# Kernel optimization log

Hardware: AMD Instinct MI355X
Metric: run time of the kernel (lower is better)

The kernel has to match this reference:

```python
import jax, jax.numpy as jnp
import numpy as np

N_NODES = 50000
IN_CH = 256
HID_CH = 64
N_EDGES = 800000


def setup_inputs() -> dict:
    key = jax.random.key(0)
    k1, k2, k3, k4, k5 = jax.random.split(key, 5)
    x = jax.random.normal(k1, (N_NODES, IN_CH), dtype=jnp.float32)
    edge_index = jax.random.randint(k2, (2, N_EDGES), 0, N_NODES, dtype=jnp.int64)
    # GCNConv linear weight (Glorot) and zero bias, as in PyG defaults
    W = jax.random.normal(k3, (IN_CH, HID_CH), dtype=jnp.float32) * (1.0 / np.sqrt(IN_CH))
    bias = jnp.zeros((HID_CH,), dtype=jnp.float32)
    # PReLU per-channel weight, torch default init 0.25
    prelu_a = jnp.full((HID_CH,), 0.25, dtype=jnp.float32)
    return {"x": x, "edge_index": edge_index, "W": W, "bias": bias, "prelu_a": prelu_a}


def reference(x, edge_index, W, bias, prelu_a):
    # GCNConv, normalize=False: transform then scatter-add over edges, + bias
    xw = x @ W                               # [N, H]
    src, dst = edge_index[0], edge_index[1]
    msgs = xw[src]                           # [E, H] gather
    agg = jax.ops.segment_sum(msgs, dst, num_segments=N_NODES)  # [N, H]
    out = agg + bias
    # per-channel PReLU
    return jnp.where(out > 0, out, prelu_a * out)
```

## Files before the change

kernel.cpp:

```cpp
#include <hip/hip_runtime.h>

#define N_NODES 50000
#define IN_CH   256
#define HID_CH  64
#define N_EDGES 800000

#define AG_ROWS 64
#define NBUCKET 782
#define CAPB    1536
#define PTILE   4096
#define NPT     196
#define GEMM_BLOCKS 391
#define CAP     2048

typedef __attribute__((ext_vector_type(8))) short short8;
typedef __attribute__((ext_vector_type(4))) float f32x4;

static __device__ __forceinline__ unsigned short f2bf(float f) {
    unsigned int u = __float_as_uint(f);
    u += 0x7FFF + ((u >> 16) & 1);
    return (unsigned short)(u >> 16);
}
static __device__ __forceinline__ float bf2f(unsigned short h) {
    return __uint_as_float(((unsigned int)h) << 16);
}

union SmemU {
    short8 wfl[2048];
    struct {
        int hcnt[NBUCKET];
        int excl[NBUCKET];
        int lcur[NBUCKET];
        int gbase[NBUCKET];
        int wsum[8];
        unsigned int staged[PTILE];
        unsigned short sbkt[PTILE];
    } p;
};

__global__ __launch_bounds__(512) void gemm_part_kernel(const float* __restrict__ x,
                                                        const float* __restrict__ W,
                                                        unsigned short* __restrict__ xwb,
                                                        const int* __restrict__ ei,
                                                        int* __restrict__ cnt,
                                                        unsigned int* __restrict__ packed_out) {
    __shared__ SmemU u;
    const int t = threadIdx.x;

    if (blockIdx.x < GEMM_BLOCKS) {
        for (int e = t; e < 2048; e += 512) {
            const int ks = e >> 8;
            const int nt = (e >> 6) & 3;
            const int l  = e & 63;
            const int q = l >> 4, m = l & 15;
            const int n = nt * 16 + m;
            const int k0 = ks * 32 + q * 8;
            short8 v;
            #pragma unroll
            for (int j = 0; j < 8; ++j) v[j] = (short)f2bf(W[(k0 + j) * HID_CH + n]);
            u.wfl[e] = v;
        }
        __syncthreads();

        const int wv = t >> 6, lane = t & 63;
        const int q = lane >> 4, m = lane & 15;
        const int row0 = blockIdx.x * 128 + wv * 16;
        const int arow = row0 + m;
        const int arl = arow < N_NODES ? arow : N_NODES - 1;
        const float* xr = x + (size_t)arl * IN_CH + q * 8;

        f32x4 acc0 = {0.f,0.f,0.f,0.f}, acc1 = acc0, acc2 = acc0, acc3 = acc0;

        #pragma unroll
        for (int ks = 0; ks < 8; ++ks) {
            const float4 a0 = *(const float4*)(xr + ks * 32);
            const float4 a1 = *(const float4*)(xr + ks * 32 + 4);
            short8 af;
            af[0] = (short)f2bf(a0.x); af[1] = (short)f2bf(a0.y);
            af[2] = (short)f2bf(a0.z); af[3] = (short)f2bf(a0.w);
            af[4] = (short)f2bf(a1.x); af[5] = (short)f2bf(a1.y);
            af[6] = (short)f2bf(a1.z); af[7] = (short)f2bf(a1.w);
            const short8 b0 = u.wfl[(ks * 4 + 0) * 64 + lane];
            const short8 b1 = u.wfl[(ks * 4 + 1) * 64 + lane];
            const short8 b2 = u.wfl[(ks * 4 + 2) * 64 + lane];
            const short8 b3 = u.wfl[(ks * 4 + 3) * 64 + lane];
            acc0 = __builtin_amdgcn_mfma_f32_16x16x32_bf16(af, b0, acc0, 0, 0, 0);
            acc1 = __builtin_amdgcn_mfma_f32_16x16x32_bf16(af, b1, acc1, 0, 0, 0);
            acc2 = __builtin_amdgcn_mfma_f32_16x16x32_bf16(af, b2, acc2, 0, 0, 0);
            acc3 = __builtin_amdgcn_mfma_f32_16x16x32_bf16(af, b3, acc3, 0, 0, 0);
        }

        #pragma unroll
        for (int r = 0; r < 4; ++r) {
            const int row = row0 + q * 4 + r;
            if (row < N_NODES) {
                unsigned short* o = xwb + (size_t)row * HID_CH + m;
                o[0]  = f2bf(acc0[r]);
                o[16] = f2bf(acc1[r]);
                o[32] = f2bf(acc2[r]);
                o[48] = f2bf(acc3[r]);
            }
        }
        return;
    }

    const int tile0 = (blockIdx.x - GEMM_BLOCKS) * PTILE;
    const int tcnt = min(PTILE, N_EDGES - tile0);

    for (int i = t; i < NBUCKET; i += 512) u.p.hcnt[i] = 0;
    __syncthreads();

    int es[8], ed[8];
    #pragma unroll
    for (int r = 0; r < 2; ++r) {
        const int base = tile0 + (r * 512 + t) * 4;
        if (base < N_EDGES) {
            const int4 s4 = *(const int4*)(ei + base);
            const int4 d4 = *(const int4*)(ei + N_EDGES + base);
            es[r*4+0] = s4.x; es[r*4+1] = s4.y; es[r*4+2] = s4.z; es[r*4+3] = s4.w;
            ed[r*4+0] = d4.x; ed[r*4+1] = d4.y; ed[r*4+2] = d4.z; ed[r*4+3] = d4.w;
        } else {
            #pragma unroll
            for (int j = 0; j < 4; ++j) es[r*4+j] = -1;
        }
    }
    #pragma unroll
    for (int i = 0; i < 8; ++i)
        if (es[i] >= 0) atomicAdd(&u.p.hcnt[ed[i] >> 6], 1);
    __syncthreads();

    const int b0 = 2 * t, b1 = 2 * t + 1;
    const int c0 = (b0 < NBUCKET) ? u.p.hcnt[b0] : 0;
    const int c1 = (b1 < NBUCKET) ? u.p.hcnt[b1] : 0;
    const int v = c0 + c1;
    int s = v;
    #pragma unroll
    for (int off = 1; off < 64; off <<= 1) {
        const int uu = __shfl_up(s, off, 64);
        if ((t & 63) >= off) s += uu;
    }
    if ((t & 63) == 63) u.p.wsum[t >> 6] = s;
    __syncthreads();
    if (t < 8) {
        const int ws = u.p.wsum[t];
        int si = ws;
        #pragma unroll
        for (int off = 1; off < 8; off <<= 1) {
            const int uu = __shfl_up(si, off, 64);
            if (t >= off) si += uu;
        }
        u.p.wsum[t] = si - ws;
    }
    __syncthreads();
    const int ex = s - v + u.p.wsum[t >> 6];
    if (b0 < NBUCKET) {
        u.p.excl[b0] = ex; u.p.lcur[b0] = ex;
        if (c0 > 0) u.p.gbase[b0] = b0 * CAPB + atomicAdd(&cnt[b0], c0);
    }
    if (b1 < NBUCKET) {
        u.p.excl[b1] = ex + c0; u.p.lcur[b1] = ex + c0;
        if (c1 > 0) u.p.gbase[b1] = b1 * CAPB + atomicAdd(&cnt[b1], c1);
    }
    __syncthreads();

    #pragma unroll
    for (int i = 0; i < 8; ++i) {
        if (es[i] >= 0) {
            const int b = ed[i] >> 6;
            const int pos = atomicAdd(&u.p.lcur[b], 1);
            u.p.staged[pos] = ((unsigned int)(ed[i] & 63) << 16) | (unsigned int)es[i];
            u.p.sbkt[pos] = (unsigned short)b;
        }
    }
    __syncthreads();

    #pragma unroll
    for (int i = 0; i < 8; ++i) {
        const int idx = t + i * 512;
        if (idx < tcnt) {
            const int b = u.p.sbkt[idx];
            packed_out[u.p.gbase[b] + (idx - u.p.excl[b])] = u.p.staged[idx];
        }
    }
}

__global__ __launch_bounds__(512) void aggregate_kernel(const unsigned short* __restrict__ xwb,
                                                        const unsigned int* __restrict__ packed,
                                                        const int* __restrict__ cnt,
                                                        const float* __restrict__ bias,
                                                        const float* __restrict__ prelu_a,
                                                        float* __restrict__ out) {
    __shared__ unsigned short ssrc[CAP];
    __shared__ int hcnt[AG_ROWS];
    __shared__ int hexcl[AG_ROWS];
    __shared__ int hcur[AG_ROWS];

    const int b = blockIdx.x;
    const int t = threadIdx.x;
    const int beg = b * CAPB;
    const int total = min(cnt[b], CAP);

    if (t < AG_ROWS) hcnt[t] = 0;
    __syncthreads();

    for (int i = t; i < total; i += 512)
        atomicAdd(&hcnt[packed[beg + i] >> 16], 1);
    __syncthreads();

    if (t < AG_ROWS) {
        const int v = hcnt[t];
        int s = v;
        #pragma unroll
        for (int off = 1; off < 64; off <<= 1) {
            const int u = __shfl_up(s, off, 64);
            if (t >= off) s += u;
        }
        hexcl[t] = s - v;
        hcur[t]  = s - v;
    }
    __syncthreads();

    for (int i = t; i < total; i += 512) {
        const unsigned int p = packed[beg + i];
        const int pos = atomicAdd(&hcur[p >> 16], 1);
        ssrc[pos] = (unsigned short)(p & 0xFFFFu);
    }
    __syncthreads();

    const int sl = t >> 3;
    const int li = t & 7;
    const int c0 = li * 8;
    const int rb = hexcl[sl];
    const int re = rb + hcnt[sl];

    float a[8];
    #pragma unroll
    for (int j = 0; j < 8; ++j) a[j] = 0.f;

    int i = rb;
    for (; i + 3 < re; i += 4) {
        const int e0 = ssrc[i + 0];
        const int e1 = ssrc[i + 1];
        const int e2 = ssrc[i + 2];
        const int e3 = ssrc[i + 3];
        const short8 v0 = *(const short8*)(xwb + (size_t)e0 * HID_CH + c0);
        const short8 v1 = *(const short8*)(xwb + (size_t)e1 * HID_CH + c0);
        const short8 v2 = *(const short8*)(xwb + (size_t)e2 * HID_CH + c0);
        const short8 v3 = *(const short8*)(xwb + (size_t)e3 * HID_CH + c0);
        #pragma unroll
        for (int j = 0; j < 8; ++j)
            a[j] += (bf2f((unsigned short)v0[j]) + bf2f((unsigned short)v1[j]))
                  + (bf2f((unsigned short)v2[j]) + bf2f((unsigned short)v3[j]));
    }
    for (; i < re; ++i) {
        const int e0 = ssrc[i];
        const short8 v0 = *(const short8*)(xwb + (size_t)e0 * HID_CH + c0);
        #pragma unroll
        for (int j = 0; j < 8; ++j) a[j] += bf2f((unsigned short)v0[j]);
    }

    const int node = b * AG_ROWS + sl;
    if (node < N_NODES) {
        const float4 bb0 = *(const float4*)(bias + c0);
        const float4 bb1 = *(const float4*)(bias + c0 + 4);
        const float4 aa0 = *(const float4*)(prelu_a + c0);
        const float4 aa1 = *(const float4*)(prelu_a + c0 + 4);
        float4 r0, r1;
        r0.x = a[0] + bb0.x; r0.x = r0.x > 0.f ? r0.x : aa0.x * r0.x;
        r0.y = a[1] + bb0.y; r0.y = r0.y > 0.f ? r0.y : aa0.y * r0.y;
        r0.z = a[2] + bb0.z; r0.z = r0.z > 0.f ? r0.z : aa0.z * r0.z;
        r0.w = a[3] + bb0.w; r0.w = r0.w > 0.f ? r0.w : aa0.w * r0.w;
        r1.x = a[4] + bb1.x; r1.x = r1.x > 0.f ? r1.x : aa1.x * r1.x;
        r1.y = a[5] + bb1.y; r1.y = r1.y > 0.f ? r1.y : aa1.y * r1.y;
        r1.z = a[6] + bb1.z; r1.z = r1.z > 0.f ? r1.z : aa1.z * r1.z;
        r1.w = a[7] + bb1.w; r1.w = r1.w > 0.f ? r1.w : aa1.w * r1.w;
        float4* op = (float4*)(out + (size_t)node * HID_CH + c0);
        op[0] = r0;
        op[1] = r1;
    }
}

extern "C" void kernel_launch(void* const* d_in, const int* in_sizes, int n_in,
                              void* d_out, int out_size, void* d_ws, size_t ws_size,
                              hipStream_t stream) {
    const float* x       = (const float*)d_in[0];
    const int*   ei      = (const int*)d_in[1];
    const float* W       = (const float*)d_in[2];
    const float* bias    = (const float*)d_in[3];
    const float* prelu_a = (const float*)d_in[4];
    float* out = (float*)d_out;

    char* w = (char*)d_ws;
    unsigned short* xwb    = (unsigned short*)(w);
    int*            cnt    = (int*)(w + 6400000);
    unsigned int*   packed = (unsigned int*)(w + 6403200);

    hipMemsetAsync(cnt, 0, NBUCKET * sizeof(int), stream);

    gemm_part_kernel<<<GEMM_BLOCKS + NPT, 512, 0, stream>>>(x, W, xwb, ei, cnt, packed);

    aggregate_kernel<<<NBUCKET, 512, 0, stream>>>(xwb, packed, cnt, bias, prelu_a, out);
}
```

Before: 125.4 us.

## Interleave GEMM and partition blocks, use hardware bf16 packing, deepen gather unroll

Interleaves edge-partition blocks with GEMM blocks by block id so that both kinds of work are co-resident across CUs. It replaces the software fp32-to-bf16 rounding with the v_cvt_pk_bf16_f32 instruction, prefetches all A rows into registers before the MFMA loop, and adds launch_bounds occupancy hint 4. It also unrolls the aggregation gather to 8 outstanding loads to raise memory-level parallelism. The trade-offs are higher register pressure and small changes to the summation order in the aggregation.

Result: no change. 125.2 us (-0.2%).

```diff
diff --git a/kernel.cpp b/kernel.cpp
--- a/kernel.cpp
+++ b/kernel.cpp
@@ -16,13 +16,13 @@
 typedef __attribute__((ext_vector_type(8))) short short8;
 typedef __attribute__((ext_vector_type(4))) float f32x4;
 
-static __device__ __forceinline__ unsigned short f2bf(float f) {
-    unsigned int u = __float_as_uint(f);
-    u += 0x7FFF + ((u >> 16) & 1);
-    return (unsigned short)(u >> 16);
-}
 static __device__ __forceinline__ float bf2f(unsigned short h) {
     return __uint_as_float(((unsigned int)h) << 16);
+}
+static __device__ __forceinline__ unsigned int cvt_pk(float lo, float hi) {
+    unsigned int r;
+    asm("v_cvt_pk_bf16_f32 %0, %1, %2" : "=v"(r) : "v"(lo), "v"(hi));
+    return r;
 }
 
 union SmemU {
@@ -38,16 +38,21 @@
     } p;
 };
 
-__global__ __launch_bounds__(512) void gemm_part_kernel(const float* __restrict__ x,
-                                                        const float* __restrict__ W,
-                                                        unsigned short* __restrict__ xwb,
-                                                        const int* __restrict__ ei,
-                                                        int* __restrict__ cnt,
-                                                        unsigned int* __restrict__ packed_out) {
+__global__ __launch_bounds__(512, 4) void gemm_part_kernel(const float* __restrict__ x,
+                                                           const float* __restrict__ W,
+                                                           unsigned short* __restrict__ xwb,
+                                                           const int* __restrict__ ei,
+                                                           int* __restrict__ cnt,
+                                                           unsigned int* __restrict__ packed_out) {
     __shared__ SmemU u;
     const int t = threadIdx.x;
-
-    if (blockIdx.x < GEMM_BLOCKS) {
+    const int bid = blockIdx.x;
+
+    int pid = -1, gid = -1;
+    if ((bid & 1) && (bid >> 1) < NPT) pid = bid >> 1;
+    else gid = (bid < 2 * NPT) ? (bid >> 1) : (bid - NPT);
+
+    if (gid >= 0) {
         for (int e = t; e < 2048; e += 512) {
             const int ks = e >> 8;
             const int nt = (e >> 6) & 3;
@@ -55,31 +60,40 @@
             const int q = l >> 4, m = l & 15;
             const int n = nt * 16 + m;
             const int k0 = ks * 32 + q * 8;
-            short8 v;
-            #pragma unroll
-            for (int j = 0; j < 8; ++j) v[j] = (short)f2bf(W[(k0 + j) * HID_CH + n]);
-            u.wfl[e] = v;
+            const float* wp = W + (size_t)k0 * HID_CH + n;
+            uint4 v;
+            v.x = cvt_pk(wp[0 * HID_CH], wp[1 * HID_CH]);
+            v.y = cvt_pk(wp[2 * HID_CH], wp[3 * HID_CH]);
+            v.z = cvt_pk(wp[4 * HID_CH], wp[5 * HID_CH]);
+            v.w = cvt_pk(wp[6 * HID_CH], wp[7 * HID_CH]);
+            ((uint4*)u.wfl)[e] = v;
         }
         __syncthreads();
 
         const int wv = t >> 6, lane = t & 63;
         const int q = lane >> 4, m = lane & 15;
-        const int row0 = blockIdx.x * 128 + wv * 16;
+        const int row0 = gid * 128 + wv * 16;
         const int arow = row0 + m;
         const int arl = arow < N_NODES ? arow : N_NODES - 1;
         const float* xr = x + (size_t)arl * IN_CH + q * 8;
 
+        float4 areg[16];
+        #pragma unroll
+        for (int ks = 0; ks < 8; ++ks) {
+            areg[2 * ks]     = *(const float4*)(xr + ks * 32);
+            areg[2 * ks + 1] = *(const float4*)(xr + ks * 32 + 4);
+        }
+
         f32x4 acc0 = {0.f,0.f,0.f,0.f}, acc1 = acc0, acc2 = acc0, acc3 = acc0;
 
         #pragma unroll
         for (int ks = 0; ks < 8; ++ks) {
-            const float4 a0 = *(const float4*)(xr + ks * 32);
-            const float4 a1 = *(const float4*)(xr + ks * 32 + 4);
             short8 af;
-            af[0] = (short)f2bf(a0.x); af[1] = (short)f2bf(a0.y);
-            af[2] = (short)f2bf(a0.z); af[3] = (short)f2bf(a0.w);
-            af[4] = (short)f2bf(a1.x); af[5] = (short)f2bf(a1.y);
-            af[6] = (short)f2bf(a1.z); af[7] = (short)f2bf(a1.w);
+            unsigned int* afu = (unsigned int*)&af;
+            afu[0] = cvt_pk(areg[2 * ks].x,     areg[2 * ks].y);
+            afu[1] = cvt_pk(areg[2 * ks].z,     areg[2 * ks].w);
+            afu[2] = cvt_pk(areg[2 * ks + 1].x, areg[2 * ks + 1].y);
+            afu[3] = cvt_pk(areg[2 * ks + 1].z, areg[2 * ks + 1].w);
             const short8 b0 = u.wfl[(ks * 4 + 0) * 64 + lane];
             const short8 b1 = u.wfl[(ks * 4 + 1) * 64 + lane];
             const short8 b2 = u.wfl[(ks * 4 + 2) * 64 + lane];
@@ -95,16 +109,18 @@
             const int row = row0 + q * 4 + r;
             if (row < N_NODES) {
                 unsigned short* o = xwb + (size_t)row * HID_CH + m;
-                o[0]  = f2bf(acc0[r]);
-                o[16] = f2bf(acc1[r]);
-                o[32] = f2bf(acc2[r]);
-                o[48] = f2bf(acc3[r]);
+                const unsigned int p01 = cvt_pk(acc0[r], acc1[r]);
+                const unsigned int p23 = cvt_pk(acc2[r], acc3[r]);
+                o[0]  = (unsigned short)(p01 & 0xFFFFu);
+                o[16] = (unsigned short)(p01 >> 16);
+                o[32] = (unsigned short)(p23 & 0xFFFFu);
+                o[48] = (unsigned short)(p23 >> 16);
             }
         }
         return;
     }
 
-    const int tile0 = (blockIdx.x - GEMM_BLOCKS) * PTILE;
+    const int tile0 = pid * PTILE;
     const int tcnt = min(PTILE, N_EDGES - tile0);
 
     for (int i = t; i < NBUCKET; i += 512) u.p.hcnt[i] = 0;
@@ -238,19 +254,31 @@
     for (int j = 0; j < 8; ++j) a[j] = 0.f;
 
     int i = rb;
+    for (; i + 7 < re; i += 8) {
+        short8 vv[8];
+        #pragma unroll
+        for (int r = 0; r < 8; ++r) {
+            const int e = ssrc[i + r];
+            vv[r] = *(const short8*)(xwb + (size_t)e * HID_CH + c0);
+        }
+        #pragma unroll
+        for (int r = 0; r < 8; ++r)
+            #pragma unroll
+            for (int j = 0; j < 8; ++j)
+                a[j] += bf2f((unsigned short)vv[r][j]);
+    }
     for (; i + 3 < re; i += 4) {
-        const int e0 = ssrc[i + 0];
-        const int e1 = ssrc[i + 1];
-        const int e2 = ssrc[i + 2];
-        const int e3 = ssrc[i + 3];
-        const short8 v0 = *(const short8*)(xwb + (size_t)e0 * HID_CH + c0);
-        const short8 v1 = *(const short8*)(xwb + (size_t)e1 * HID_CH + c0);
-        const short8 v2 = *(const short8*)(xwb + (size_t)e2 * HID_CH + c0);
-        const short8 v3 = *(const short8*)(xwb + (size_t)e3 * HID_CH + c0);
-        #pragma unroll
-        for (int j = 0; j < 8; ++j)
-            a[j] += (bf2f((unsigned short)v0[j]) + bf2f((unsigned short)v1[j]))
-                  + (bf2f((unsigned short)v2[j]) + bf2f((unsigned short)v3[j]));
+        short8 vv[4];
+        #pragma unroll
+        for (int r = 0; r < 4; ++r) {
+            const int e = ssrc[i + r];
+            vv[r] = *(const short8*)(xwb + (size_t)e * HID_CH + c0);
+        }
+        #pragma unroll
+        for (int r = 0; r < 4; ++r)
+            #pragma unroll
+            for (int j = 0; j < 8; ++j)
+                a[j] += bf2f((unsigned short)vv[r][j]);
     }
     for (; i < re; ++i) {
         const int e0 = ssrc[i];
```
